# Performance work log

Hardware: AMD Instinct MI355X
Metric: run time of the kernel (lower is better)

## Reference

```python
import jax, jax.numpy as jnp
from jax import lax
import numpy as np

H, W = 240, 304
IN_CH, OUT_CH, K = 16, 32, 3
B = 8
N_PER = 65536
N = B * N_PER
CIN = IN_CH + 2  # pos + neg + features


def setup_inputs() -> dict:
    key = jax.random.key(0)
    k1, k2, k3, k4, k5 = jax.random.split(key, 5)
    # events columns: x, y, t in [0,1); polarity in {0,1}
    xyt = jax.random.uniform(k1, (N, 3), dtype=jnp.float32)
    pol = jax.random.randint(k2, (N, 1), 0, 2).astype(jnp.float32)
    events = jnp.concatenate([xyt, pol], axis=1)
    features = jax.random.normal(k3, (N, IN_CH), dtype=jnp.float32)
    offsets = (jnp.arange(1, B + 1, dtype=jnp.int64) * N_PER)  # cumulative counts
    # SubmanifoldConvolution params: one [CIN, OUT_CH] matrix per filter offset -> HWIO
    fan_in = K * K * CIN
    weight = jax.random.normal(k4, (K, K, CIN, OUT_CH), dtype=jnp.float32) / np.sqrt(fan_in)
    bias = jax.random.normal(k5, (OUT_CH,), dtype=jnp.float32) * 0.01
    return {"events": events, "features": features, "weight": weight,
            "bias": bias, "offsets": offsets}


def reference(events, features, weight, bias, offsets):
    n = events.shape[0]
    b = offsets.shape[0]
    # offset2batch: row i belongs to first sample whose cumulative offset exceeds i
    batch = jnp.searchsorted(offsets, jnp.arange(n, dtype=offsets.dtype), side="right").astype(jnp.int32)
    pos = events[:, 3:4]
    neg = 1.0 - pos
    sparse = jnp.concatenate([pos, neg, features], axis=1)  # [N, CIN]
    # yx = events[:, [1, 0]] scaled by (h, w), rounded to grid coords
    yi = jnp.clip(jnp.round(events[:, 1] * H).astype(jnp.int32), 0, H - 1)
    xi = jnp.clip(jnp.round(events[:, 0] * W).astype(jnp.int32), 0, W - 1)
    key = (batch * H + yi) * W + xi  # linear site id, [N]
    nseg = b * H * W
    # scn InputLayer mode=4: average features of duplicate coordinates
    feat_sum = jax.ops.segment_sum(sparse, key, num_segments=nseg)  # [nseg, CIN]
    cnt = jax.ops.segment_sum(jnp.ones((n,), sparse.dtype), key, num_segments=nseg)
    dense = feat_sum / jnp.maximum(cnt, 1.0)[:, None]
    dense = dense.reshape(b, H, W, CIN)  # zeros at inactive sites
    # Submanifold 3x3 conv: inactive neighbors are zero, so a dense SAME conv
    # evaluated only at active sites matches the submanifold rulebook math.
    out = lax.conv_general_dilated(dense, weight, window_strides=(1, 1),
                                   padding="SAME",
                                   dimension_numbers=("NHWC", "HWIO", "NHWC"))
    out = out.reshape(nseg, OUT_CH)
    # OutputLayer: read back per input row (active sites only), add bias there
    f = out[key] + bias  # [N, OUT_CH]
    return f
```

## Files before the change

kernel.cpp:

```cpp
#include <hip/hip_runtime.h>

#define Hh 240
#define Ww 304
#define IN_CH 16
#define OUT_CH 32
#define Bb 8
#define N_PER 65536
#define N_EV (Bb * N_PER)
#define CIN (IN_CH + 2)
#define NSEG (Bb * Hh * Ww)
#define NBLK 570

#define DP 10

#define TW 32
#define TH 8
#define HW_ 34
#define HH_ 10
#define NXT_TILES 10
#define NYT_TILES 30
#define OPITCH 33
#define HALO_DW (HH_ * HW_ * DP)
#define HALO_LD 3424

typedef __attribute__((ext_vector_type(8))) short bf16x8;
typedef __attribute__((ext_vector_type(4))) float f32x4;

__device__ __forceinline__ unsigned short f2bf(float x) {
  unsigned u = __float_as_uint(x);
  unsigned r = u + 0x7fffu + ((u >> 16) & 1u);
  return (unsigned short)(r >> 16);
}
__device__ __forceinline__ float bf2f(unsigned short b) {
  return __uint_as_float(((unsigned)b) << 16);
}
__device__ __forceinline__ unsigned pk2(float a, float b) {
  return (unsigned)f2bf(a) | ((unsigned)f2bf(b) << 16);
}

__global__ __launch_bounds__(256) void hist_rank_kernel(
    const float* __restrict__ events, const int* __restrict__ offsets,
    int* __restrict__ hist, int2* __restrict__ kr) {
  int i = blockIdx.x * blockDim.x + threadIdx.x;
  float4 ev = ((const float4*)events)[i];
  int yi = (int)rintf(ev.y * (float)Hh);
  yi = min(max(yi, 0), Hh - 1);
  int xi = (int)rintf(ev.x * (float)Ww);
  xi = min(max(xi, 0), Ww - 1);
  int b = 0;
#pragma unroll
  for (int j = 0; j < Bb; j++) b += (offsets[j] <= i) ? 1 : 0;
  int key = (b * Hh + yi) * Ww + xi;
  int pol = (ev.w != 0.0f) ? 1 : 0;
  int rank = atomicAdd(&hist[key], 1);
  kr[i] = make_int2(key | (pol << 31), rank);
}

__global__ __launch_bounds__(256) void scan1_kernel(int* __restrict__ data,
                                                    int* __restrict__ blockSum) {
  __shared__ int lds[256];
  int b = blockIdx.x, t = threadIdx.x;
  int idx = b * 1024 + t * 4;
  int4 v = *(const int4*)(data + idx);
  int s0 = v.x, s1 = s0 + v.y, s2 = s1 + v.z, s3 = s2 + v.w;
  lds[t] = s3;
  __syncthreads();
  int val = s3;
  for (int off = 1; off < 256; off <<= 1) {
    int n = (t >= off) ? lds[t - off] : 0;
    __syncthreads();
    val += n;
    lds[t] = val;
    __syncthreads();
  }
  int excl = val - s3;
  int4 o;
  o.x = excl; o.y = excl + s0; o.z = excl + s1; o.w = excl + s2;
  *(int4*)(data + idx) = o;
  if (t == 255) blockSum[b] = val;
}

__global__ __launch_bounds__(1024) void scan2_weights_kernel(
    const int* __restrict__ blockSum, int* __restrict__ blockOffset,
    const float* __restrict__ weight, unsigned short* __restrict__ wprep) {
  int t = threadIdx.x;
  if (blockIdx.x == 1) {
#pragma unroll
    for (int it = 0; it < 6; it++) {
      int idx = it * 1024 + t;
      int ky = idx >> 11;
      int rem = idx & 2047;
      int n = rem >> 6;
      int kl = rem & 63;
      unsigned short v = 0;
      if (kl < 60) {
        int kx = kl / 20, ci = kl - kx * 20;
        if (ci < 18) v = f2bf(weight[((ky * 3 + kx) * CIN + ci) * OUT_CH + n]);
      }
      wprep[idx] = v;
    }
    return;
  }
  __shared__ int lds[1024];
  int v = (t < NBLK) ? blockSum[t] : 0;
  lds[t] = v;
  __syncthreads();
  int val = v;
  for (int off = 1; off < 1024; off <<= 1) {
    int n = (t >= off) ? lds[t - off] : 0;
    __syncthreads();
    val += n;
    lds[t] = val;
    __syncthreads();
  }
  if (t < NBLK) blockOffset[t] = val - v;
  if (t == 0) blockOffset[NBLK] = lds[1023];
}

__global__ __launch_bounds__(256) void scatter_rec_kernel(
    const float* __restrict__ features, const int2* __restrict__ kr,
    const int* __restrict__ baseLocal, const int* __restrict__ blockOffset,
    uint4* __restrict__ sortedRec, int* __restrict__ sortedMeta) {
  int i = blockIdx.x * blockDim.x + threadIdx.x;
  int2 m = kr[i];
  int key = m.x & 0x7fffffff;
  int pos = baseLocal[key] + blockOffset[key >> 10] + m.y;
  float pol = (float)(((unsigned)m.x) >> 31);
  const float4* f = (const float4*)(features + (size_t)i * IN_CH);
  float4 f0 = f[0], f1 = f[1], f2 = f[2], f3 = f[3];
  uint4* R = sortedRec + (size_t)pos * 4;
  R[0] = make_uint4(pk2(pol, 1.0f - pol), pk2(f0.x, f0.y), pk2(f0.z, f0.w),
                    pk2(f1.x, f1.y));
  R[1] = make_uint4(pk2(f1.z, f1.w), pk2(f2.x, f2.y), pk2(f2.z, f2.w),
                    pk2(f3.x, f3.y));
  R[2] = make_uint4(pk2(f3.z, f3.w), 0, 0, 0);
  R[3] = make_uint4(0, 0, 0, 0);
  sortedMeta[pos] = i;
}

__global__ __launch_bounds__(256) void densify_kernel(
    const uint4* __restrict__ sortedRec, const int* __restrict__ baseLocal,
    const int* __restrict__ blockOffset, unsigned* __restrict__ dense) {
  int p = blockIdx.x * 256 + threadIdx.x;
  int bo = blockOffset[p >> 10];
  int base = baseLocal[p] + bo;
  int nxt = ((p & 1023) != 1023) ? (baseLocal[p + 1] + bo)
                                 : blockOffset[(p >> 10) + 1];
  int c = nxt - base;
  float acc[CIN];
#pragma unroll
  for (int k = 0; k < CIN; k++) acc[k] = 0.0f;
  for (int j = 0; j < c; j++) {
    const uint4* R = sortedRec + (size_t)(base + j) * 4;
    uint4 r0 = R[0], r1 = R[1];
    unsigned d8 = ((const unsigned*)R)[8];
    acc[0]  += bf2f((unsigned short)r0.x);  acc[1]  += bf2f((unsigned short)(r0.x >> 16));
    acc[2]  += bf2f((unsigned short)r0.y);  acc[3]  += bf2f((unsigned short)(r0.y >> 16));
    acc[4]  += bf2f((unsigned short)r0.z);  acc[5]  += bf2f((unsigned short)(r0.z >> 16));
    acc[6]  += bf2f((unsigned short)r0.w);  acc[7]  += bf2f((unsigned short)(r0.w >> 16));
    acc[8]  += bf2f((unsigned short)r1.x);  acc[9]  += bf2f((unsigned short)(r1.x >> 16));
    acc[10] += bf2f((unsigned short)r1.y);  acc[11] += bf2f((unsigned short)(r1.y >> 16));
    acc[12] += bf2f((unsigned short)r1.z);  acc[13] += bf2f((unsigned short)(r1.z >> 16));
    acc[14] += bf2f((unsigned short)r1.w);  acc[15] += bf2f((unsigned short)(r1.w >> 16));
    acc[16] += bf2f((unsigned short)d8);    acc[17] += bf2f((unsigned short)(d8 >> 16));
  }
  float inv = 1.0f / fmaxf((float)c, 1.0f);
  unsigned* dp = dense + (size_t)p * DP;
#pragma unroll
  for (int k = 0; k < 9; k++) dp[k] = pk2(acc[2 * k] * inv, acc[2 * k + 1] * inv);
  dp[9] = 0;
}

__global__ __launch_bounds__(256) void fused_conv_kernel(
    const unsigned* __restrict__ dense, const int* __restrict__ sortedMeta,
    const int* __restrict__ baseLocal, const int* __restrict__ blockOffset,
    const unsigned short* __restrict__ wprep, const float* __restrict__ bias,
    float* __restrict__ out) {
  __shared__ unsigned smem[128 * OPITCH];

  int blk = blockIdx.x;
  int xt = blk % NXT_TILES;
  int rem = blk / NXT_TILES;
  int yt = rem % NYT_TILES;
  int b = rem / NYT_TILES;
  int x0 = xt * TW, y0 = yt * TH;
  int tid = threadIdx.x;

  int tx = tid & 31, ty = tid >> 5;
  int gxo = x0 + tx;
  int c = 0, base = 0;
  if (gxo < Ww) {
    int p = (b * Hh + y0 + ty) * Ww + gxo;
    int bo = blockOffset[p >> 10];
    base = baseLocal[p] + bo;
    int nxt = ((p & 1023) != 1023) ? (baseLocal[p + 1] + bo)
                                   : blockOffset[(p >> 10) + 1];
    c = nxt - base;
  }
  int m0 = (c > 0) ? sortedMeta[base] : 0;

  for (int i = tid; i < HALO_LD; i += 256) {
    int r = i / 340;
    int cd = i - r * 340;
    int hx = cd / 10;
    int k = cd - hx * 10;
    int gy = y0 - 1 + r, gx = x0 - 1 + hx;
    unsigned v = 0;
    if (gy >= 0 && gy < Hh && gx >= 0 && gx < Ww)
      v = dense[(size_t)((b * Hh + gy) * Ww + gx) * DP + k];
    smem[i] = v;
  }
  __syncthreads();

  int wv = tid >> 6, lane = tid & 63;
  int quad = lane >> 4, lrow = lane & 15;

  f32x4 accf[4][2];
#pragma unroll
  for (int i = 0; i < 4; i++)
#pragma unroll
    for (int nt = 0; nt < 2; nt++) accf[i][nt] = (f32x4){0.f, 0.f, 0.f, 0.f};

  const unsigned* hp = smem;
#pragma unroll
  for (int ky = 0; ky < 3; ky++) {
    bf16x8 bfr[2][2];
#pragma unroll
    for (int kh = 0; kh < 2; kh++)
#pragma unroll
      for (int nt = 0; nt < 2; nt++) {
        int n = nt * 16 + lrow;
        bfr[kh][nt] = *(const bf16x8*)(wprep + ((ky * 32 + n) << 6) +
                                       kh * 32 + quad * 8);
      }
#pragma unroll
    for (int i = 0; i < 4; i++) {
      int t0 = (wv * 4 + i) * 16;
      int ox = (t0 & 31) + lrow;
      int oy = t0 >> 5;
      int pix = (oy + ky) * HW_ + ox;
#pragma unroll
      for (int kh = 0; kh < 2; kh++) {
        union { bf16x8 v; unsigned u[4]; } a;
        int ui = pix * DP + kh * 16 + quad * 4;
        a.u[0] = hp[ui]; a.u[1] = hp[ui + 1];
        a.u[2] = hp[ui + 2]; a.u[3] = hp[ui + 3];
        accf[i][0] = __builtin_amdgcn_mfma_f32_16x16x32_bf16(
            a.v, bfr[kh][0], accf[i][0], 0, 0, 0);
        accf[i][1] = __builtin_amdgcn_mfma_f32_16x16x32_bf16(
            a.v, bfr[kh][1], accf[i][1], 0, 0, 0);
      }
    }
  }
  __syncthreads();

  float* outsh = (float*)smem;
  float bn0 = bias[lrow], bn1 = bias[16 + lrow];
#pragma unroll
  for (int ch = 0; ch < 2; ch++) {
#pragma unroll
    for (int ii = 0; ii < 2; ii++) {
      int i = ch * 2 + ii;
      int lidx = ii * 16 + quad * 4;
      int row = wv * 32 + lidx;
#pragma unroll
      for (int r = 0; r < 4; r++) {
        outsh[(row + r) * OPITCH + lrow] = accf[i][0][r] + bn0;
        outsh[(row + r) * OPITCH + 16 + lrow] = accf[i][1][r] + bn1;
      }
    }
    __syncthreads();
    if (((tid >> 5) & 1) == ch && gxo < Ww && c > 0) {
      int row = (tid >> 6) * 32 + ((tid & 63) - ch * 32);
      const float* rp = outsh + row * OPITCH;
      float4 o0 = make_float4(rp[0], rp[1], rp[2], rp[3]);
      float4 o1 = make_float4(rp[4], rp[5], rp[6], rp[7]);
      float4 o2 = make_float4(rp[8], rp[9], rp[10], rp[11]);
      float4 o3 = make_float4(rp[12], rp[13], rp[14], rp[15]);
      float4 o4 = make_float4(rp[16], rp[17], rp[18], rp[19]);
      float4 o5 = make_float4(rp[20], rp[21], rp[22], rp[23]);
      float4 o6 = make_float4(rp[24], rp[25], rp[26], rp[27]);
      float4 o7 = make_float4(rp[28], rp[29], rp[30], rp[31]);
      for (int j = 0; j < c; j++) {
        int ev = (j == 0) ? m0 : sortedMeta[base + j];
        float4* op = (float4*)(out + (size_t)ev * OUT_CH);
        op[0] = o0; op[1] = o1; op[2] = o2; op[3] = o3;
        op[4] = o4; op[5] = o5; op[6] = o6; op[7] = o7;
      }
    }
    __syncthreads();
  }
}

extern "C" void kernel_launch(void* const* d_in, const int* in_sizes, int n_in,
                              void* d_out, int out_size, void* d_ws,
                              size_t ws_size, hipStream_t stream) {
  const float* events = (const float*)d_in[0];
  const float* features = (const float*)d_in[1];
  const float* weight = (const float*)d_in[2];
  const float* bias = (const float*)d_in[3];
  const int* offsets = (const int*)d_in[4];
  float* out = (float*)d_out;

  uint4* sortedRec = (uint4*)d_ws;
  unsigned* dense = (unsigned*)(sortedRec + (size_t)N_EV * 4);
  int* sortedMeta = (int*)(dense + (size_t)NSEG * DP);
  int2* kr = (int2*)(sortedMeta + N_EV);
  int* hist = (int*)(kr + N_EV);
  int* blockOffset = hist + NSEG;
  int* blockSum = blockOffset + 1024;
  unsigned short* wprep = (unsigned short*)(blockSum + 1024);

  hipMemsetAsync(hist, 0, (size_t)NSEG * sizeof(int), stream);

  hist_rank_kernel<<<N_EV / 256, 256, 0, stream>>>(events, offsets, hist, kr);
  scan1_kernel<<<NBLK, 256, 0, stream>>>(hist, blockSum);
  scan2_weights_kernel<<<2, 1024, 0, stream>>>(blockSum, blockOffset, weight,
                                               wprep);
  scatter_rec_kernel<<<N_EV / 256, 256, 0, stream>>>(
      features, kr, hist, blockOffset, sortedRec, sortedMeta);
  densify_kernel<<<NSEG / 256, 256, 0, stream>>>(sortedRec, hist, blockOffset,
                                                 dense);
  fused_conv_kernel<<<Bb * NYT_TILES * NXT_TILES, 256, 0, stream>>>(
      dense, sortedMeta, hist, blockOffset, wprep, bias, out);
}
```

Baseline: 206.2 us.

## Cooperative coalesced output scatter using per-row event ranges and packed x coordinate

Packs each event's grid x coordinate into the high bits of sortedMeta so the conv kernel can map sorted events back to tile pixels. Output writing changes from one thread per pixel looping over its duplicate events to groups of 8 threads per event, each writing one float4, iterating over the contiguous sorted range for each tile row. This balances work across threads and makes each event's 128-byte output row a single coalesced store, at the cost of more shared-memory reads and index arithmetic.

New measurement: 201.5 us. 2.3% less time.

```diff
diff --git a/kernel.cpp b/kernel.cpp
--- a/kernel.cpp
+++ b/kernel.cpp
@@ -135,7 +135,8 @@
                     pk2(f3.x, f3.y));
   R[2] = make_uint4(pk2(f3.z, f3.w), 0, 0, 0);
   R[3] = make_uint4(0, 0, 0, 0);
-  sortedMeta[pos] = i;
+  int x = key % Ww;
+  sortedMeta[pos] = i | (x << 19);
 }
 
 __global__ __launch_bounds__(256) void densify_kernel(
@@ -177,6 +178,7 @@
     const unsigned short* __restrict__ wprep, const float* __restrict__ bias,
     float* __restrict__ out) {
   __shared__ unsigned smem[128 * OPITCH];
+  __shared__ int rowRg[TH][2];
 
   int blk = blockIdx.x;
   int xt = blk % NXT_TILES;
@@ -188,16 +190,18 @@
 
   int tx = tid & 31, ty = tid >> 5;
   int gxo = x0 + tx;
-  int c = 0, base = 0;
+  int xlast = min(x0 + TW - 1, Ww - 1);
   if (gxo < Ww) {
     int p = (b * Hh + y0 + ty) * Ww + gxo;
     int bo = blockOffset[p >> 10];
-    base = baseLocal[p] + bo;
-    int nxt = ((p & 1023) != 1023) ? (baseLocal[p + 1] + bo)
-                                   : blockOffset[(p >> 10) + 1];
-    c = nxt - base;
-  }
-  int m0 = (c > 0) ? sortedMeta[base] : 0;
+    int base = baseLocal[p] + bo;
+    if (tx == 0) rowRg[ty][0] = base;
+    if (gxo == xlast) {
+      int nxt = ((p & 1023) != 1023) ? (baseLocal[p + 1] + bo)
+                                     : blockOffset[(p >> 10) + 1];
+      rowRg[ty][1] = nxt;
+    }
+  }
 
   for (int i = tid; i < HALO_LD; i += 256) {
     int r = i / 340;
@@ -270,22 +274,21 @@
       }
     }
     __syncthreads();
-    if (((tid >> 5) & 1) == ch && gxo < Ww && c > 0) {
-      int row = (tid >> 6) * 32 + ((tid & 63) - ch * 32);
-      const float* rp = outsh + row * OPITCH;
-      float4 o0 = make_float4(rp[0], rp[1], rp[2], rp[3]);
-      float4 o1 = make_float4(rp[4], rp[5], rp[6], rp[7]);
-      float4 o2 = make_float4(rp[8], rp[9], rp[10], rp[11]);
-      float4 o3 = make_float4(rp[12], rp[13], rp[14], rp[15]);
-      float4 o4 = make_float4(rp[16], rp[17], rp[18], rp[19]);
-      float4 o5 = make_float4(rp[20], rp[21], rp[22], rp[23]);
-      float4 o6 = make_float4(rp[24], rp[25], rp[26], rp[27]);
-      float4 o7 = make_float4(rp[28], rp[29], rp[30], rp[31]);
-      for (int j = 0; j < c; j++) {
-        int ev = (j == 0) ? m0 : sortedMeta[base + j];
-        float4* op = (float4*)(out + (size_t)ev * OUT_CH);
-        op[0] = o0; op[1] = o1; op[2] = o2; op[3] = o3;
-        op[4] = o4; op[5] = o5; op[6] = o6; op[7] = o7;
+    int lq = tid & 7;
+    int grp = tid >> 3;
+#pragma unroll
+    for (int rr = 0; rr < 4; rr++) {
+      int ty2 = ch + rr * 2;
+      int rS = rowRg[ty2][0], rE = rowRg[ty2][1];
+      for (int s = grp; s < rE - rS; s += 32) {
+        unsigned meta = (unsigned)sortedMeta[rS + s];
+        int ev = meta & 0x7FFFF;
+        int lx = (int)((meta >> 19) & 0x1FF) - x0;
+        int pid = ty2 * 32 + lx;
+        int orow = ((pid >> 6) << 5) + (((pid >> 4) & 1) << 4) + (pid & 15);
+        const float* rp = outsh + orow * OPITCH + (lq << 2);
+        float4 v = make_float4(rp[0], rp[1], rp[2], rp[3]);
+        ((float4*)(out + (size_t)ev * OUT_CH))[lq] = v;
       }
     }
     __syncthreads();
```
